# Kernel tuning notes

Measured on AMD Instinct MI355X. Metric: run time of the kernel, lower is better.

The kernel has to match this reference:

```python
import jax, jax.numpy as jnp
import numpy as np

MAX_L = 6
L = MAX_L + 1  # internal self.max_l in the torch module
N = 2_000_000


def _sph_constants(Lmax):
    lm = np.arange(Lmax)
    ls = lm * lm
    pt = np.zeros((Lmax, Lmax), dtype=np.int64)
    yr = np.zeros((Lmax, Lmax), dtype=np.int64)
    yr_rev = np.zeros((Lmax, Lmax), dtype=np.int64)
    num_lm = (Lmax + 1) * Lmax // 2
    ca = np.zeros(num_lm, dtype=np.float64)
    cb = np.zeros(num_lm, dtype=np.float64)
    for l in range(Lmax):
        m = np.arange(l + 1)
        pt[l, : l + 1] = m + l * (l + 1) // 2
        yr[l, : l + 1] = ls[l] + l + m
        yr_rev[l, : l + 1] = ls[l] + l - m
        if l > 0:
            ca[pt[l, :l]] = np.sqrt((4.0 * ls[l] - 1.0) / (ls[l] - ls[:l]))
            cb[pt[l, :l]] = -np.sqrt((ls[l - 1] - ls[:l]) / (4.0 * ls[l - 1] - 1.0))
    p1 = -np.sqrt(1.0 + 0.5 / np.maximum(lm, 1))  # prefactor1; index 0 unused
    p2 = np.sqrt(2.0 * lm + 3.0)                  # prefactor2
    return pt, yr, yr_rev, ca, cb, p1, p2

_PT, _YR, _YRR, _CA, _CB, _P1, _P2 = _sph_constants(L)
_SQRT2_REV = float(np.sqrt(0.5))
_SQRT2PI_REV = float(np.sqrt(0.5 / np.pi))
_HC1 = float(np.sqrt(15.0 / (4.0 * np.pi)))
_HC2 = float(np.sqrt(5.0 / (16.0 * np.pi)))
_HC3 = float(np.sqrt(15.0 / (16.0 * np.pi)))


def setup_inputs() -> dict:
    key = jax.random.key(0)
    cart = jax.random.normal(key, (3, N), dtype=jnp.float32)
    return {"cart": cart}


def _sph_forward(cart):
    dt = cart.dtype
    x, y, z = cart[0], cart[1], cart[2]
    d_sq = x * x + y * y + z * z  # == norm(cart, axis=0)**2
    nb = x.ndim  # number of trailing batch dims (here 1)

    sph = [None] * (L * L)
    sph[0] = jnp.full(x.shape, _SQRT2PI_REV * _SQRT2_REV, dtype=dt)
    sph[1] = (_P1[1] * _SQRT2PI_REV) * y
    sph[2] = (_P2[0] * _SQRT2_REV * _SQRT2PI_REV) * z
    sph[3] = (_P1[1] * _SQRT2PI_REV) * x
    # l = 2 hard-coded block
    sph[4] = _HC1 * x * y
    sph[5] = -_HC1 * y * z
    sph[6] = _HC2 * (3.0 * z * z - d_sq)
    sph[7] = -_HC1 * x * z
    sph[8] = _HC3 * (x * x - y * y)

    for l in range(3, L):
        # vectorized band over m = 0..l-2 (positive-m / yr branch)
        a = jnp.asarray(_CA[_PT[l, : l - 1]], dt).reshape((l - 1,) + (1,) * nb)
        b = jnp.asarray(_CB[_PT[l, : l - 1]], dt).reshape((l - 1,) + (1,) * nb)
        prev = jnp.stack([sph[int(_YR[l - 1, m])] for m in range(l - 1)])
        prev2 = jnp.stack([sph[int(_YR[l - 2, m])] for m in range(l - 1)])
        blk = a * (z * prev + b * d_sq * prev2)
        for m in range(l - 1):
            sph[int(_YR[l, m])] = blk[m]
        # negative-m / yr_rev branch over m = 1..l-2
        if l - 1 > 1:
            a2 = jnp.asarray(_CA[_PT[l, 1 : l - 1]], dt).reshape((l - 2,) + (1,) * nb)
            b2 = jnp.asarray(_CB[_PT[l, 1 : l - 1]], dt).reshape((l - 2,) + (1,) * nb)
            prev_r = jnp.stack([sph[int(_YRR[l - 1, m])] for m in range(1, l - 1)])
            prev2_r = jnp.stack([sph[int(_YRR[l - 2, m])] for m in range(1, l - 1)])
            blk_r = a2 * (z * prev_r + b2 * d_sq * prev2_r)
            for i, m in enumerate(range(1, l - 1)):
                sph[int(_YRR[l, m])] = blk_r[i]
        # edge terms m = l-1 and m = l
        top_p = sph[int(_YR[l - 1, l - 1])]
        top_n = sph[int(_YRR[l - 1, l - 1])]
        sph[int(_YR[l, l - 1])] = _P2[l - 1] * z * top_p
        sph[int(_YRR[l, l - 1])] = _P2[l - 1] * z * top_n
        sph[int(_YR[l, l])] = _P1[l] * (x * top_p - y * top_n)
        sph[int(_YRR[l, l])] = _P1[l] * (x * top_n + y * top_p)

    return jnp.stack(sph)  # (L*L, ...batch)


def reference(cart):
    return _sph_forward(cart)
```

## Files before the change

kernel.cpp:

```cpp
#include <hip/hip_runtime.h>

constexpr double csqrt(double x) {
    double r = x > 1.0 ? x : 1.0;
    for (int i = 0; i < 60; ++i) r = 0.5 * (r + x / r);
    return r;
}

constexpr double PI_D    = 3.14159265358979323846264338327950288;
constexpr double SQ2R    = csqrt(0.5);
constexpr double SQ2PIR  = csqrt(0.5 / PI_D);
constexpr double C00_D   = SQ2PIR * SQ2R;
constexpr double C1Y_D   = -csqrt(1.5) * SQ2PIR;

struct SphConsts {
    double ca[7][7];
    double cb[7][7];
    double p1[7];
    double p2[7];
};

constexpr SphConsts makeConsts() {
    SphConsts c{};
    for (int l = 1; l < 7; ++l) {
        for (int m = 0; m < l; ++m) {
            c.ca[l][m] = csqrt((4.0 * l * l - 1.0) / (double)(l * l - m * m));
            double num = (double)((l - 1) * (l - 1) - m * m);
            double den = 4.0 * (l - 1) * (l - 1) - 1.0;
            c.cb[l][m] = -csqrt(num / den < 0.0 ? 0.0 : num / den);
        }
        c.p1[l] = -csqrt(1.0 + 0.5 / (double)l);
    }
    for (int l = 0; l < 7; ++l) c.p2[l] = csqrt(2.0 * l + 3.0);
    return c;
}

constexpr SphConsts CC = makeConsts();

typedef float f4 __attribute__((ext_vector_type(4)));

__device__ __forceinline__ void stv(float* p, float v) {
    __builtin_nontemporal_store(v, p);
}
__device__ __forceinline__ void stv(float* p, f4 v) {
    __builtin_nontemporal_store(v, reinterpret_cast<f4*>(p));
}

template <typename T> __device__ __forceinline__ T bcast(float v);
template <> __device__ __forceinline__ float bcast<float>(float v) { return v; }
template <> __device__ __forceinline__ f4    bcast<f4>(float v)    { f4 t = {v, v, v, v}; return t; }

template <typename T>
__device__ __forceinline__ void sph_point(T x, T y, T z, float* __restrict__ o, size_t N) {
    const T d2 = x * x + y * y + z * z;

    T pa = bcast<T>((float)C00_D);
    stv(o + 0 * N, pa);
    T pb = (float)CC.p2[0] * (z * pa);
    stv(o + 2 * N, pb);
#pragma unroll
    for (int l = 2; l <= 6; ++l) {
        const float a = (float)CC.ca[l][0];
        const float b = (float)CC.cb[l][0];
        T pc = a * (z * pb + b * (d2 * pa));
        stv(o + (size_t)(l * l + l) * N, pc);
        pa = pb; pb = pc;
    }

    T dp = (float)C1Y_D * x;
    T dn = (float)C1Y_D * y;
    stv(o + 3 * N, dp);
    stv(o + 1 * N, dn);

#pragma unroll
    for (int m = 1; m <= 6; ++m) {
        if (m >= 2) {
            const float p1v = (float)CC.p1[m];
            T ndp = p1v * (x * dp - y * dn);
            T ndn = p1v * (x * dn + y * dp);
            dp = ndp; dn = ndn;
            stv(o + (size_t)(m * m + 2 * m) * N, dp);
            stv(o + (size_t)(m * m) * N, dn);
        }
        if (m <= 5) {
            const float p2v = (float)CC.p2[m];
            T qp = p2v * (z * dp);
            T qn = p2v * (z * dn);
            {
                const int l = m + 1;
                stv(o + (size_t)(l * l + l + m) * N, qp);
                stv(o + (size_t)(l * l + l - m) * N, qn);
            }
            T ap = dp, bp = qp, an = dn, bn = qn;
#pragma unroll
            for (int l = m + 2; l <= 6; ++l) {
                const float a = (float)CC.ca[l][m];
                const float b = (float)CC.cb[l][m];
                T cp = a * (z * bp + b * (d2 * ap));
                T cn = a * (z * bn + b * (d2 * an));
                stv(o + (size_t)(l * l + l + m) * N, cp);
                stv(o + (size_t)(l * l + l - m) * N, cn);
                ap = bp; bp = cp;
                an = bn; bn = cn;
            }
        }
    }
}

template <typename T, int W>
__global__ void sph_kernel(const float* __restrict__ cart,
                           float* __restrict__ out, int N) {
    const int i = blockIdx.x * blockDim.x + threadIdx.x;
    const int nW = N / W;
    if (i >= nW) return;
    const size_t sN = (size_t)N;
    const float* p = cart + (size_t)W * i;
    T X = *reinterpret_cast<const T*>(p);
    T Y = *reinterpret_cast<const T*>(p + sN);
    T Z = *reinterpret_cast<const T*>(p + 2 * sN);
    sph_point<T>(X, Y, Z, out + (size_t)W * i, sN);
}

extern "C" void kernel_launch(void* const* d_in, const int* in_sizes, int n_in,
                              void* d_out, int out_size, void* d_ws, size_t ws_size,
                              hipStream_t stream) {
    const float* cart = (const float*)d_in[0];
    float* out = (float*)d_out;
    const int N = in_sizes[0] / 3;

    const int threads = 256;
    if ((N & 3) == 0) {
        const int n4 = N >> 2;
        const int blocks = (n4 + threads - 1) / threads;
        sph_kernel<f4, 4><<<blocks, threads, 0, stream>>>(cart, out, N);
    } else {
        const int blocks = (N + threads - 1) / threads;
        sph_kernel<float, 1><<<blocks, threads, 0, stream>>>(cart, out, N);
    }
}
```

Before: 75.68 us.

## Split spherical harmonics into two kernels by degree range

The work is split into two launches. The first writes degrees 0-4 and the second recomputes the recurrences up to degree 6 but stores only degrees 5-6. The likely aim is to lower register pressure or spread the write streams across two passes. In exchange, cart is read twice, the low-degree recurrences are recomputed, and a second launch is added.

```diff
diff --git a/kernel.cpp b/kernel.cpp
--- a/kernel.cpp
+++ b/kernel.cpp
@@ -49,56 +49,62 @@
 template <> __device__ __forceinline__ float bcast<float>(float v) { return v; }
 template <> __device__ __forceinline__ f4    bcast<f4>(float v)    { f4 t = {v, v, v, v}; return t; }
 
-template <typename T>
+template <typename T, int LTOP, int LMIN>
 __device__ __forceinline__ void sph_point(T x, T y, T z, float* __restrict__ o, size_t N) {
     const T d2 = x * x + y * y + z * z;
 
     T pa = bcast<T>((float)C00_D);
-    stv(o + 0 * N, pa);
+    if (0 >= LMIN) stv(o + 0 * N, pa);
     T pb = (float)CC.p2[0] * (z * pa);
-    stv(o + 2 * N, pb);
+    if (1 >= LMIN) stv(o + 2 * N, pb);
 #pragma unroll
-    for (int l = 2; l <= 6; ++l) {
+    for (int l = 2; l <= LTOP; ++l) {
         const float a = (float)CC.ca[l][0];
         const float b = (float)CC.cb[l][0];
         T pc = a * (z * pb + b * (d2 * pa));
-        stv(o + (size_t)(l * l + l) * N, pc);
+        if (l >= LMIN) stv(o + (size_t)(l * l + l) * N, pc);
         pa = pb; pb = pc;
     }
 
     T dp = (float)C1Y_D * x;
     T dn = (float)C1Y_D * y;
-    stv(o + 3 * N, dp);
-    stv(o + 1 * N, dn);
+    if (1 >= LMIN) {
+        stv(o + 3 * N, dp);
+        stv(o + 1 * N, dn);
+    }
 
 #pragma unroll
-    for (int m = 1; m <= 6; ++m) {
+    for (int m = 1; m <= LTOP; ++m) {
         if (m >= 2) {
             const float p1v = (float)CC.p1[m];
             T ndp = p1v * (x * dp - y * dn);
             T ndn = p1v * (x * dn + y * dp);
             dp = ndp; dn = ndn;
-            stv(o + (size_t)(m * m + 2 * m) * N, dp);
-            stv(o + (size_t)(m * m) * N, dn);
+            if (m >= LMIN) {
+                stv(o + (size_t)(m * m + 2 * m) * N, dp);
+                stv(o + (size_t)(m * m) * N, dn);
+            }
         }
-        if (m <= 5) {
+        if (m + 1 <= LTOP) {
             const float p2v = (float)CC.p2[m];
             T qp = p2v * (z * dp);
             T qn = p2v * (z * dn);
-            {
+            if (m + 1 >= LMIN) {
                 const int l = m + 1;
                 stv(o + (size_t)(l * l + l + m) * N, qp);
                 stv(o + (size_t)(l * l + l - m) * N, qn);
             }
             T ap = dp, bp = qp, an = dn, bn = qn;
 #pragma unroll
-            for (int l = m + 2; l <= 6; ++l) {
+            for (int l = m + 2; l <= LTOP; ++l) {
                 const float a = (float)CC.ca[l][m];
                 const float b = (float)CC.cb[l][m];
                 T cp = a * (z * bp + b * (d2 * ap));
                 T cn = a * (z * bn + b * (d2 * an));
-                stv(o + (size_t)(l * l + l + m) * N, cp);
-                stv(o + (size_t)(l * l + l - m) * N, cn);
+                if (l >= LMIN) {
+                    stv(o + (size_t)(l * l + l + m) * N, cp);
+                    stv(o + (size_t)(l * l + l - m) * N, cn);
+                }
                 ap = bp; bp = cp;
                 an = bn; bn = cn;
             }
@@ -106,7 +112,7 @@
     }
 }
 
-template <typename T, int W>
+template <typename T, int W, int LTOP, int LMIN>
 __global__ void sph_kernel(const float* __restrict__ cart,
                            float* __restrict__ out, int N) {
     const int i = blockIdx.x * blockDim.x + threadIdx.x;
@@ -117,7 +123,7 @@
     T X = *reinterpret_cast<const T*>(p);
     T Y = *reinterpret_cast<const T*>(p + sN);
     T Z = *reinterpret_cast<const T*>(p + 2 * sN);
-    sph_point<T>(X, Y, Z, out + (size_t)W * i, sN);
+    sph_point<T, LTOP, LMIN>(X, Y, Z, out + (size_t)W * i, sN);
 }
 
 extern "C" void kernel_launch(void* const* d_in, const int* in_sizes, int n_in,
@@ -131,9 +137,11 @@
     if ((N & 3) == 0) {
         const int n4 = N >> 2;
         const int blocks = (n4 + threads - 1) / threads;
-        sph_kernel<f4, 4><<<blocks, threads, 0, stream>>>(cart, out, N);
+        sph_kernel<f4, 4, 4, 0><<<blocks, threads, 0, stream>>>(cart, out, N);
+        sph_kernel<f4, 4, 6, 5><<<blocks, threads, 0, stream>>>(cart, out, N);
     } else {
         const int blocks = (N + threads - 1) / threads;
-        sph_kernel<float, 1><<<blocks, threads, 0, stream>>>(cart, out, N);
+        sph_kernel<float, 1, 4, 0><<<blocks, threads, 0, stream>>>(cart, out, N);
+        sph_kernel<float, 1, 6, 5><<<blocks, threads, 0, stream>>>(cart, out, N);
     }
 }
```

Measured after the change: 76.45 us. No clear change (+1.0%).
